# Kernel tuning notes

Measured on AMD Instinct MI355X. Metric: run time of the kernel, lower is better.

## Reference

```python
import jax, jax.numpy as jnp
import numpy as np
from jax import lax


def _sobel_weights():
    kx = np.array([[[1, 0, -1], [1, 0, -1], [1, 0, -1]],
                   [[2, 0, -2], [2, 0, -2], [2, 0, -2]],
                   [[1, 0, -1], [1, 0, -1], [1, 0, -1]]], dtype=np.float32)
    ky = np.array([[[1, 2, 1], [1, 2, 1], [1, 2, 1]],
                   [[0, 0, 0], [0, 0, 0], [0, 0, 0]],
                   [[-1, -2, -1], [-1, -2, -1], [-1, -2, -1]]], dtype=np.float32)
    kz = np.array([[[1, 2, 1], [0, 0, 0], [-1, -2, -1]],
                   [[1, 2, 1], [0, 0, 0], [-1, -2, -1]],
                   [[1, 2, 1], [0, 0, 0], [-1, -2, -1]]], dtype=np.float32)
    # [O=3, I=1, 3, 3, 3]: all three directional stencils in a single conv
    return jnp.asarray(np.stack([kx, ky, kz])[:, None])


def setup_inputs() -> dict:
    key = jax.random.key(0)
    data = jax.random.uniform(key, (4, 1, 256, 256, 64), dtype=jnp.float32)
    return {"data": data, "weight": _sobel_weights()}


def reference(data, weight):
    # data: [B,1,D,H,W]; weight: [3,1,3,3,3]
    x = jnp.where(data == 255.0, 0.0, data)
    # torch Conv3d is cross-correlation, matching lax.conv_general_dilated
    grad = lax.conv_general_dilated(
        x, weight, window_strides=(1, 1, 1), padding="SAME",
        dimension_numbers=("NCDHW", "OIDHW", "NCDHW"))  # [B,3,D,H,W]
    # dx/dy/dz thresholding: any nonzero gradient becomes 1 (else stays 0)
    b = (jnp.abs(grad) > 0).astype(x.dtype)
    # channel-wise L2 norm of binarized gradients, then threshold at 1
    norm = jnp.sqrt(jnp.sum(b * b, axis=1, keepdims=True))  # [B,1,D,H,W]
    return (norm > 1.0).astype(x.dtype)
```

## Files before the change

kernel.cpp:

```cpp
#include <hip/hip_runtime.h>


constexpr int DDIM = 256;
constexpr int HDIM = 256;
constexpr int WWID = 64;
constexpr int DC   = 8;
constexpr int HT   = 8;

typedef float vfloat4 __attribute__((ext_vector_type(4)));

struct P3  { float ds[4], ss[4], sd[4]; };
struct Raw { float4 a, b, c; };

__device__ __forceinline__ float dpp_up1(float v) {
  return __builtin_bit_cast(float, __builtin_amdgcn_update_dpp(
      0, __builtin_bit_cast(int, v), 0x111, 0xf, 0xf, true));
}
__device__ __forceinline__ float dpp_dn1(float v) {
  return __builtin_bit_cast(float, __builtin_amdgcn_update_dpp(
      0, __builtin_bit_cast(int, v), 0x101, 0xf, 0xf, true));
}

__global__ __launch_bounds__(128) void sobel3d_kernel(
    const float* __restrict__ in, float* __restrict__ out) {
  const int lane = threadIdx.x;
  const int wg   = lane & 15;
  const int hs   = lane >> 4;
  const int w0   = wg * 4;
  const int h    = blockIdx.x * HT + threadIdx.y * 4 + hs;
  const int d0   = blockIdx.y * DC;
  const int b    = blockIdx.z;

  const size_t plane = (size_t)HDIM * WWID;
  const float* src = in  + (size_t)b * DDIM * plane;
  float*       dst = out + (size_t)b * DDIM * plane;

  const size_t offb = (size_t)h * WWID + w0;
  const bool va = (h > 0);
  const bool vc = (h + 1 < HDIM);

  auto loadPlane = [&](int d, Raw& r) {
    if ((unsigned)d < (unsigned)DDIM) {
      const float* p = src + (size_t)d * plane;
      r.b = *(const float4*)(p + offb);
      r.a = va ? *(const float4*)(p + offb - WWID) : float4{0.f, 0.f, 0.f, 0.f};
      r.c = vc ? *(const float4*)(p + offb + WWID) : float4{0.f, 0.f, 0.f, 0.f};
    } else {
      r.a = r.b = r.c = float4{0.f, 0.f, 0.f, 0.f};
    }
  };

  auto rowSD = [&](float4 v, float* S, float* D) {
    const float x1 = (v.x == 255.f) ? 0.f : v.x;
    const float x2 = (v.y == 255.f) ? 0.f : v.y;
    const float x3 = (v.z == 255.f) ? 0.f : v.z;
    const float x4 = (v.w == 255.f) ? 0.f : v.w;
    const float xm = dpp_up1(x4);
    const float xp = dpp_dn1(x1);
    const float x[6] = {xm, x1, x2, x3, x4, xp};
    #pragma unroll
    for (int i = 0; i < 4; ++i) {
      S[i] = fmaf(2.f, x[i + 1], x[i]) + x[i + 2];
      D[i] = x[i] - x[i + 2];
    }
  };

  auto partials = [&](const Raw& r, P3& o) {
    float Sa[4], Da[4], Sb[4], Db[4], Sc[4], Dc[4];
    rowSD(r.a, Sa, Da);
    rowSD(r.b, Sb, Db);
    rowSD(r.c, Sc, Dc);
    #pragma unroll
    for (int i = 0; i < 4; ++i) {
      o.ds[i] = Da[i] + Db[i] + Dc[i];
      o.ss[i] = Sa[i] + Sb[i] + Sc[i];
      o.sd[i] = Sa[i] - Sc[i];
    }
  };

  auto emit = [&](int d, const P3& p, const P3& c, const P3& n) {
    vfloat4 o;
    #pragma unroll
    for (int i = 0; i < 4; ++i) {
      const float Gx = fmaf(2.f, c.ds[i], p.ds[i]) + n.ds[i];
      const float Gy = p.ss[i] - n.ss[i];
      const float Gz = p.sd[i] + c.sd[i] + n.sd[i];
      const int cnt = (Gx != 0.f) + (Gy != 0.f) + (Gz != 0.f);
      o[i] = (cnt >= 2) ? 1.f : 0.f;
    }
    __builtin_nontemporal_store(o, (vfloat4*)(dst + (size_t)d * plane + offb));
  };

  Raw A, B, C, D;
  P3 p0, p1, p2;

  loadPlane(d0 - 1, A);
  loadPlane(d0,     B);
  loadPlane(d0 + 1, C);
  loadPlane(d0 + 2, D);
  partials(A, p0);  loadPlane(d0 + 3, A);
  partials(B, p1);  loadPlane(d0 + 4, B);
  partials(C, p2);  emit(d0,     p0, p1, p2);  loadPlane(d0 + 5, C);
  partials(D, p0);  emit(d0 + 1, p1, p2, p0);  loadPlane(d0 + 6, D);
  partials(A, p1);  emit(d0 + 2, p2, p0, p1);  loadPlane(d0 + 7, A);
  partials(B, p2);  emit(d0 + 3, p0, p1, p2);  loadPlane(d0 + 8, B);
  partials(C, p0);  emit(d0 + 4, p1, p2, p0);
  partials(D, p1);  emit(d0 + 5, p2, p0, p1);
  partials(A, p2);  emit(d0 + 6, p0, p1, p2);
  partials(B, p0);  emit(d0 + 7, p1, p2, p0);
}

extern "C" void kernel_launch(void* const* d_in, const int* in_sizes, int n_in,
                              void* d_out, int out_size, void* d_ws, size_t ws_size,
                              hipStream_t stream) {
  const float* data = (const float*)d_in[0];
  float* out = (float*)d_out;
  dim3 grid(HDIM / HT, DDIM / DC, 4);
  dim3 block(WWID, 2);
  sobel3d_kernel<<<grid, block, 0, stream>>>(data, out);
}
```

Before: 32.30 us.

## Compute two H rows per thread to share vertical loads and partials

Each thread now produces two adjacent H rows instead of one, loading four rows per plane instead of three and sharing the middle-row sums between both outputs. This cuts redundant global loads per output and halves the grid size. The prefetch depth drops from four planes to three to contain register pressure, and the nontemporal stores become plain stores. The risks are reduced latency hiding from the shallower prefetch and fewer blocks to fill the GPU.

```diff
diff --git a/kernel.cpp b/kernel.cpp
--- a/kernel.cpp
+++ b/kernel.cpp
@@ -5,12 +5,12 @@
 constexpr int HDIM = 256;
 constexpr int WWID = 64;
 constexpr int DC   = 8;
-constexpr int HT   = 8;
+constexpr int HT   = 16;
 
 typedef float vfloat4 __attribute__((ext_vector_type(4)));
 
-struct P3  { float ds[4], ss[4], sd[4]; };
-struct Raw { float4 a, b, c; };
+struct Raw { float4 a, b, c, d; };
+struct P3  { float ds0[4], ds1[4], ss0[4], ss1[4], sd0[4], sd1[4]; };
 
 __device__ __forceinline__ float dpp_up1(float v) {
   return __builtin_bit_cast(float, __builtin_amdgcn_update_dpp(
@@ -27,7 +27,7 @@
   const int wg   = lane & 15;
   const int hs   = lane >> 4;
   const int w0   = wg * 4;
-  const int h    = blockIdx.x * HT + threadIdx.y * 4 + hs;
+  const int hb   = blockIdx.x * HT + threadIdx.y * 8 + hs * 2;
   const int d0   = blockIdx.y * DC;
   const int b    = blockIdx.z;
 
@@ -35,18 +35,19 @@
   const float* src = in  + (size_t)b * DDIM * plane;
   float*       dst = out + (size_t)b * DDIM * plane;
 
-  const size_t offb = (size_t)h * WWID + w0;
-  const bool va = (h > 0);
-  const bool vc = (h + 1 < HDIM);
+  const size_t offb = (size_t)hb * WWID + w0;
+  const bool va = (hb > 0);
+  const bool vd = (hb + 2 < HDIM);
 
   auto loadPlane = [&](int d, Raw& r) {
     if ((unsigned)d < (unsigned)DDIM) {
       const float* p = src + (size_t)d * plane;
       r.b = *(const float4*)(p + offb);
-      r.a = va ? *(const float4*)(p + offb - WWID) : float4{0.f, 0.f, 0.f, 0.f};
-      r.c = vc ? *(const float4*)(p + offb + WWID) : float4{0.f, 0.f, 0.f, 0.f};
+      r.c = *(const float4*)(p + offb + WWID);
+      r.a = va ? *(const float4*)(p + offb - WWID)     : float4{0.f, 0.f, 0.f, 0.f};
+      r.d = vd ? *(const float4*)(p + offb + 2 * WWID) : float4{0.f, 0.f, 0.f, 0.f};
     } else {
-      r.a = r.b = r.c = float4{0.f, 0.f, 0.f, 0.f};
+      r.a = r.b = r.c = r.d = float4{0.f, 0.f, 0.f, 0.f};
     }
   };
 
@@ -66,48 +67,64 @@
   };
 
   auto partials = [&](const Raw& r, P3& o) {
-    float Sa[4], Da[4], Sb[4], Db[4], Sc[4], Dc[4];
+    float Sa[4], Da[4], Sb[4], Db[4], Sc[4], Dc[4], Sd[4], Dd[4];
     rowSD(r.a, Sa, Da);
     rowSD(r.b, Sb, Db);
     rowSD(r.c, Sc, Dc);
+    rowSD(r.d, Sd, Dd);
     #pragma unroll
     for (int i = 0; i < 4; ++i) {
-      o.ds[i] = Da[i] + Db[i] + Dc[i];
-      o.ss[i] = Sa[i] + Sb[i] + Sc[i];
-      o.sd[i] = Sa[i] - Sc[i];
+      const float D12 = Db[i] + Dc[i];
+      const float S12 = Sb[i] + Sc[i];
+      o.ds0[i] = Da[i] + D12;
+      o.ds1[i] = D12 + Dd[i];
+      o.ss0[i] = Sa[i] + S12;
+      o.ss1[i] = S12 + Sd[i];
+      o.sd0[i] = Sa[i] - Sc[i];
+      o.sd1[i] = Sb[i] - Sd[i];
     }
   };
 
   auto emit = [&](int d, const P3& p, const P3& c, const P3& n) {
-    vfloat4 o;
+    vfloat4 o0, o1;
     #pragma unroll
     for (int i = 0; i < 4; ++i) {
-      const float Gx = fmaf(2.f, c.ds[i], p.ds[i]) + n.ds[i];
-      const float Gy = p.ss[i] - n.ss[i];
-      const float Gz = p.sd[i] + c.sd[i] + n.sd[i];
-      const int cnt = (Gx != 0.f) + (Gy != 0.f) + (Gz != 0.f);
-      o[i] = (cnt >= 2) ? 1.f : 0.f;
+      {
+        const float Gx = fmaf(2.f, c.ds0[i], p.ds0[i]) + n.ds0[i];
+        const float Gy = p.ss0[i] - n.ss0[i];
+        const float Gz = p.sd0[i] + c.sd0[i] + n.sd0[i];
+        const int cnt = (Gx != 0.f) + (Gy != 0.f) + (Gz != 0.f);
+        o0[i] = (cnt >= 2) ? 1.f : 0.f;
+      }
+      {
+        const float Gx = fmaf(2.f, c.ds1[i], p.ds1[i]) + n.ds1[i];
+        const float Gy = p.ss1[i] - n.ss1[i];
+        const float Gz = p.sd1[i] + c.sd1[i] + n.sd1[i];
+        const int cnt = (Gx != 0.f) + (Gy != 0.f) + (Gz != 0.f);
+        o1[i] = (cnt >= 2) ? 1.f : 0.f;
+      }
     }
-    __builtin_nontemporal_store(o, (vfloat4*)(dst + (size_t)d * plane + offb));
+    float* q = dst + (size_t)d * plane + offb;
+    *(vfloat4*)q = o0;
+    *(vfloat4*)(q + WWID) = o1;
   };
 
-  Raw A, B, C, D;
+  Raw A, B, C;
   P3 p0, p1, p2;
 
   loadPlane(d0 - 1, A);
   loadPlane(d0,     B);
   loadPlane(d0 + 1, C);
-  loadPlane(d0 + 2, D);
-  partials(A, p0);  loadPlane(d0 + 3, A);
-  partials(B, p1);  loadPlane(d0 + 4, B);
-  partials(C, p2);  emit(d0,     p0, p1, p2);  loadPlane(d0 + 5, C);
-  partials(D, p0);  emit(d0 + 1, p1, p2, p0);  loadPlane(d0 + 6, D);
-  partials(A, p1);  emit(d0 + 2, p2, p0, p1);  loadPlane(d0 + 7, A);
-  partials(B, p2);  emit(d0 + 3, p0, p1, p2);  loadPlane(d0 + 8, B);
-  partials(C, p0);  emit(d0 + 4, p1, p2, p0);
-  partials(D, p1);  emit(d0 + 5, p2, p0, p1);
-  partials(A, p2);  emit(d0 + 6, p0, p1, p2);
-  partials(B, p0);  emit(d0 + 7, p1, p2, p0);
+  partials(A, p0);  loadPlane(d0 + 2, A);
+  partials(B, p1);  loadPlane(d0 + 3, B);
+  partials(C, p2);  emit(d0,     p0, p1, p2);  loadPlane(d0 + 4, C);
+  partials(A, p0);  emit(d0 + 1, p1, p2, p0);  loadPlane(d0 + 5, A);
+  partials(B, p1);  emit(d0 + 2, p2, p0, p1);  loadPlane(d0 + 6, B);
+  partials(C, p2);  emit(d0 + 3, p0, p1, p2);  loadPlane(d0 + 7, C);
+  partials(A, p0);  emit(d0 + 4, p1, p2, p0);  loadPlane(d0 + 8, A);
+  partials(B, p1);  emit(d0 + 5, p2, p0, p1);
+  partials(C, p2);  emit(d0 + 6, p0, p1, p2);
+  partials(A, p0);  emit(d0 + 7, p1, p2, p0);
 }
 
 extern "C" void kernel_launch(void* const* d_in, const int* in_sizes, int n_in,
```

Result: no change. 31.68 us (-1.9%).
